# Performance work log

Measured on AMD Instinct MI355X. Metric: run time of the kernel, lower is better.

The kernel has to match this reference:

```python
import jax, jax.numpy as jnp
import numpy as np

NH, DK, DV, D = 8, 64, 64, 768
DECAY = 0.95
WRITE_STRENGTH = 0.1


def setup_inputs() -> dict:
    key = jax.random.key(0)
    ks = jax.random.split(key, 6)
    s = 0.02  # small init scale for projection weights
    return {
        "x": jax.random.normal(ks[0], (4, 4096, D), dtype=jnp.float32),
        "w_key": jax.random.normal(ks[1], (NH * DK, D), dtype=jnp.float32) * s,
        "w_value": jax.random.normal(ks[2], (NH * DV, D), dtype=jnp.float32) * s,
        "w_query": jax.random.normal(ks[3], (NH * DK, D), dtype=jnp.float32) * s,
        "w_gate": jax.random.normal(ks[4], (NH, D), dtype=jnp.float32) * s,
        "w_out": jax.random.normal(ks[5], (D, NH * DV), dtype=jnp.float32) * s,
    }


def reference(x, w_key, w_value, w_query, w_gate, w_out):
    B, S, _ = x.shape
    # Batched projections (torch Linear: y = x @ W.T)
    k = (x @ w_key.T).reshape(B, S, NH, DK)
    v = (x @ w_value.T).reshape(B, S, NH, DV)
    q = (x @ w_query.T).reshape(B, S, NH, DK)
    gate = jax.nn.sigmoid(x @ w_gate.T)  # (B, S, NH)

    # Writes only use batch element 0 (mirrors k[0], v[0], gate[0] in source)
    k0 = k[0]      # (S, NH, DK)
    v0 = v[0]      # (S, NH, DV)
    g0 = gate[0]   # (S, NH)

    def step(fw, inp):
        q_t, k0_t, v0_t, g0_t = inp
        # Read BEFORE this step's decay+write
        retrieved = jnp.einsum('bhk,hkv->bhv', q_t, fw)  # (B, NH, DV)
        write = (WRITE_STRENGTH * g0_t)[:, None, None] * (k0_t[:, :, None] * v0_t[:, None, :])
        fw_new = DECAY * fw + jax.lax.stop_gradient(write)
        return fw_new, retrieved

    fw0 = jnp.zeros((NH, DK, DV), dtype=x.dtype)
    inputs = (q.transpose(1, 0, 2, 3), k0, v0, g0)  # time-major
    _, retrieved = jax.lax.scan(step, fw0, inputs)   # (S, B, NH, DV)
    retrieved = retrieved.transpose(1, 0, 2, 3).reshape(B, S, NH * DV)
    return x + retrieved @ w_out.T
```

## Files before the change

### kernel.cpp

```cpp
#include <hip/hip_runtime.h>
#include <hip/hip_bf16.h>

typedef __hip_bfloat16 bf16;
typedef __attribute__((ext_vector_type(8))) short   bf16x8;
typedef __attribute__((ext_vector_type(4))) float   f32x4;

#define B_   4
#define S_   4096
#define D_   768
#define NH_  8
#define DK_  64
#define DV_  64
#define CH_  64
#define NCH_ (S_/CH_)
#define DECAY_ 0.95f
#define WSTR_  0.1f

__device__ __forceinline__ float b2f(bf16 v) { return __bfloat162float(v); }
__device__ __forceinline__ bf16  f2b(float v) { return __float2bfloat16(v); }

__device__ __forceinline__ void gl2lds16(const bf16* g, bf16* lds) {
    __builtin_amdgcn_global_load_lds(
        (const __attribute__((address_space(1))) void*)g,
        (__attribute__((address_space(3))) void*)lds, 16, 0, 0);
}

__global__ __launch_bounds__(192) void cast_gate(const float* __restrict__ x,
                                                 bf16* __restrict__ xb,
                                                 const float* __restrict__ wg,
                                                 float* __restrict__ wgt) {
    const int s = blockIdx.x;
    const int tid = threadIdx.x;
    const float4 v = *reinterpret_cast<const float4*>(x + (size_t)s * D_ + tid * 4);
    union { bf16 b4[4]; ushort4 u; } t;
    t.b4[0] = f2b(v.x); t.b4[1] = f2b(v.y); t.b4[2] = f2b(v.z); t.b4[3] = f2b(v.w);
    *reinterpret_cast<ushort4*>(xb + (size_t)s * D_ + tid * 4) = t.u;

    if (s < S_) {
        __shared__ float red[3 * 8];
        float p[8];
        const float* wgp = wg + tid * 4;
        #pragma unroll
        for (int h = 0; h < 8; h++) {
            const float4 wv = *reinterpret_cast<const float4*>(wgp + h * D_);
            p[h] = v.x * wv.x + v.y * wv.y + v.z * wv.z + v.w * wv.w;
        }
        #pragma unroll
        for (int h = 0; h < 8; h++)
            #pragma unroll
            for (int off = 32; off; off >>= 1) p[h] += __shfl_down(p[h], off);
        const int w = tid >> 6, lane = tid & 63;
        if (lane == 0) {
            #pragma unroll
            for (int h = 0; h < 8; h++) red[w * 8 + h] = p[h];
        }
        __syncthreads();
        if (tid < 8) {
            const float sum = red[tid] + red[8 + tid] + red[16 + tid];
            wgt[s * NH_ + tid] = WSTR_ / (1.f + expf(-sum));
        }
    }
}

__global__ __launch_bounds__(256) void cast_w4(const float* __restrict__ wq,
                                               const float* __restrict__ wk,
                                               const float* __restrict__ wv,
                                               const float* __restrict__ wo,
                                               bf16* __restrict__ dq, bf16* __restrict__ dk,
                                               bf16* __restrict__ dv, bf16* __restrict__ dob) {
    const int which = blockIdx.x / 384, b = blockIdx.x % 384;
    const float* src = which == 0 ? wq : which == 1 ? wk : which == 2 ? wv : wo;
    bf16*       dst = which == 0 ? dq : which == 1 ? dk : which == 2 ? dv : dob;
    const int i = (b * 256 + threadIdx.x) * 4;
    const float4 v = *reinterpret_cast<const float4*>(src + i);
    union { bf16 b4[4]; ushort4 u; } t;
    t.b4[0] = f2b(v.x); t.b4[1] = f2b(v.y); t.b4[2] = f2b(v.z); t.b4[3] = f2b(v.w);
    *reinterpret_cast<ushort4*>(dst + i) = t.u;
}

template<typename TC, int ADDX, int KV>
__global__ __launch_bounds__(256) void gemm_mfma(const bf16* __restrict__ A,
                                                 const bf16* __restrict__ B0,
                                                 const bf16* __restrict__ B1,
                                                 const float* __restrict__ X,
                                                 TC* __restrict__ C0,
                                                 TC* __restrict__ C1,
                                                 int M, int N, int K, int nb0) {
    __shared__ bf16 As[128 * 32];
    __shared__ bf16 Bs[128 * 32];
    int bx, by;
    {
        const int gx = gridDim.x, gy = gridDim.y;
        const int L = blockIdx.y * gx + blockIdx.x;
        if ((gy & 7) == 0) {
            const int rpx = gy >> 3;
            const int xcd = L & 7;
            const int i   = L >> 3;
            by = xcd * rpx + i / gx;
            bx = i % gx;
        } else { bx = blockIdx.x; by = blockIdx.y; }
    }
    const bf16* Bm = B0;
    TC* C = C0;
    if (KV && bx >= nb0) { Bm = B1; C = C1; bx -= nb0; }
    const int bm = by * 128, bn = bx * 128;
    const int tid = threadIdx.x, lane = tid & 63, w = tid >> 6;
    const int quad = lane >> 4, l16 = lane & 15;
    const int wm = (w >> 1) * 64, wn = (w & 1) * 64;

    int ro[2], ko[2];
    #pragma unroll
    for (int c = 0; c < 2; c++) {
        const int o = (w * 2 + c) * 1024 + lane * 16;
        ro[c] = o >> 6;
        ko[c] = (o & 63) >> 1;
    }

    f32x4 acc[4][4] = {};

    for (int k0 = 0; k0 < K; k0 += 32) {
        #pragma unroll
        for (int c = 0; c < 2; c++) {
            bf16* lA = &As[(w * 2 + c) * 512];
            bf16* lB = &Bs[(w * 2 + c) * 512];
            gl2lds16(A  + (size_t)(bm + ro[c]) * K + k0 + ko[c], lA);
            gl2lds16(Bm + (size_t)(bn + ro[c]) * K + k0 + ko[c], lB);
        }
        __syncthreads();
        bf16x8 af[4], bfr[4];
        #pragma unroll
        for (int t = 0; t < 4; t++) {
            af[t]  = *reinterpret_cast<const bf16x8*>(&As[(wm + t * 16 + l16) * 32 + quad * 8]);
            bfr[t] = *reinterpret_cast<const bf16x8*>(&Bs[(wn + t * 16 + l16) * 32 + quad * 8]);
        }
        #pragma unroll
        for (int mt = 0; mt < 4; mt++)
            #pragma unroll
            for (int nt = 0; nt < 4; nt++)
                acc[mt][nt] = __builtin_amdgcn_mfma_f32_16x16x32_bf16(
                    af[mt], bfr[nt], acc[mt][nt], 0, 0, 0);
        __syncthreads();
    }

    #pragma unroll
    for (int mt = 0; mt < 4; mt++)
        #pragma unroll
        for (int nt = 0; nt < 4; nt++)
            #pragma unroll
            for (int r = 0; r < 4; r++) {
                const int m = bm + wm + mt * 16 + quad * 4 + r;
                const int n = bn + wn + nt * 16 + l16;
                float v = acc[mt][nt][r];
                if (ADDX) v += X[(size_t)m * N + n];
                if (sizeof(TC) == 2) *(bf16*)&C[(size_t)m * N + n] = f2b(v);
                else                 *(float*)&C[(size_t)m * N + n] = v;
            }
}

__global__ __launch_bounds__(256) void chunk_sums(const bf16* __restrict__ k0,
                                                  const bf16* __restrict__ v0,
                                                  const float* __restrict__ wgt,
                                                  bf16* __restrict__ lsumsT) {
    const int n = blockIdx.x, h = blockIdx.y;
    __shared__ float ks[CH_][65];
    __shared__ float vs[CH_][64];
    __shared__ float cw[CH_];
    const int tid = threadIdx.x;
    for (int e = tid; e < CH_ * 64; e += 256) {
        const int r = e >> 6, c = e & 63;
        const int t = n * CH_ + r;
        ks[r][c] = b2f(k0[(size_t)t * (NH_ * DK_) + h * DK_ + c]);
        vs[r][c] = b2f(v0[(size_t)t * (NH_ * DV_) + h * DV_ + c]);
    }
    if (tid < CH_) {
        const int t = n * CH_ + tid;
        cw[tid] = powf(DECAY_, (float)(CH_ - 1 - tid)) * wgt[t * NH_ + h];
    }
    __syncthreads();
    const int j = tid & 63, ig = tid >> 6;
    float acc[16] = {};
    for (int idx = 0; idx < CH_; idx++) {
        const float ck = cw[idx] * ks[idx][j];
        #pragma unroll
        for (int r = 0; r < 16; r++) acc[r] += vs[idx][ig * 16 + r] * ck;
    }
    bf16* out = lsumsT + ((size_t)(n * NH_ + h)) * (DK_ * DV_);
    #pragma unroll
    for (int r = 0; r < 16; r++) out[(ig * 16 + r) * 64 + j] = f2b(acc[r]);
}

__global__ __launch_bounds__(256) void state_scan(const bf16* __restrict__ lsumsT,
                                                  bf16* __restrict__ statesT) {
    const int h = blockIdx.x >> 4;
    const int e = (blockIdx.x & 15) * 256 + threadIdx.x;
    const float dC = powf(DECAY_, (float)CH_);
    float fw = 0.f;
    for (int n = 0; n < NCH_; n++) {
        const size_t idx = ((size_t)(n * NH_ + h)) * (DK_ * DV_) + e;
        statesT[idx] = f2b(fw);
        fw = dC * fw + b2f(lsumsT[idx]);
    }
}

__global__ __launch_bounds__(256) void chunk_output(const bf16* __restrict__ q,
                                                    const bf16* __restrict__ k0,
                                                    const bf16* __restrict__ v0,
                                                    const float* __restrict__ wgt,
                                                    const bf16* __restrict__ statesT,
                                                    bf16* __restrict__ retr) {
    const int n = blockIdx.x, h = blockIdx.y, b = blockIdx.z;
    __shared__ bf16 QsVT[64 * 72];
    __shared__ bf16 KsAm[64 * 72];
    __shared__ bf16 FWT[64 * 64];
    __shared__ float dpow[64], winv[64];
    const int tid = threadIdx.x, lane = tid & 63, w = tid >> 6;
    const int quad = lane >> 4, l16 = lane & 15;
    const int t0 = n * CH_;

    #pragma unroll
    for (int c = 0; c < 2; c++) {
        const int seg = w * 2 + c;
        const int row = seg * 8 + (lane >> 3);
        const int col = (lane & 7) * 8;
        gl2lds16(q  + ((size_t)(b * S_ + t0 + row)) * 512 + h * 64 + col, &QsVT[seg * 512]);
        gl2lds16(k0 + ((size_t)(t0 + row)) * 512 + h * 64 + col,          &KsAm[seg * 512]);
        gl2lds16(statesT + ((size_t)(n * NH_ + h)) * 4096 + seg * 512 + lane * 8, &FWT[seg * 512]);
    }
    ushort4 vreg[4];
    const int jb = (tid & 15) * 4;
    const int sb = tid >> 4;
    #pragma unroll
    for (int it = 0; it < 4; it++) {
        vreg[it] = *reinterpret_cast<const ushort4*>(
            v0 + ((size_t)(t0 + sb + it * 16)) * 512 + h * 64 + jb);
    }
    if (tid < 64) {
        dpow[tid] = powf(DECAY_, (float)tid);
        winv[tid] = wgt[(t0 + tid) * NH_ + h] * powf(DECAY_, -(float)(tid + 1));
    }
    __syncthreads();

    const int mrow = w * 16;
    float dpow_tt[4], winv_l[4];
    #pragma unroll
    for (int r = 0; r < 4; r++) dpow_tt[r] = dpow[mrow + quad * 4 + r];
    #pragma unroll
    for (int nt = 0; nt < 4; nt++) winv_l[nt] = winv[nt * 16 + l16];

    const bf16x8 af0 = *reinterpret_cast<const bf16x8*>(&QsVT[(mrow + l16) * 64 + quad * 8]);
    const bf16x8 af1 = *reinterpret_cast<const bf16x8*>(&QsVT[(mrow + l16) * 64 + 32 + quad * 8]);
    f32x4 acc[4] = {};
    #pragma unroll
    for (int nt = 0; nt < 4; nt++) {
        const bf16x8 b0 = *reinterpret_cast<const bf16x8*>(&KsAm[(nt * 16 + l16) * 64 + quad * 8]);
        const bf16x8 b1 = *reinterpret_cast<const bf16x8*>(&KsAm[(nt * 16 + l16) * 64 + 32 + quad * 8]);
        acc[nt] = __builtin_amdgcn_mfma_f32_16x16x32_bf16(af0, b0, acc[nt], 0, 0, 0);
        acc[nt] = __builtin_amdgcn_mfma_f32_16x16x32_bf16(af1, b1, acc[nt], 0, 0, 0);
    }
    __syncthreads();

    #pragma unroll
    for (int nt = 0; nt < 4; nt++) {
        const int s = nt * 16 + l16;
        #pragma unroll
        for (int r = 0; r < 4; r++) {
            const int tt = mrow + quad * 4 + r;
            const float v = (s < tt) ? acc[nt][r] * dpow_tt[r] * winv_l[nt] : 0.f;
            KsAm[tt * 72 + s] = f2b(v);
        }
    }
    {
        ushort* VT = reinterpret_cast<ushort*>(QsVT);
        #pragma unroll
        for (int it = 0; it < 4; it++) {
            const int s = sb + it * 16;
            VT[(jb + 0) * 72 + s] = vreg[it].x;
            VT[(jb + 1) * 72 + s] = vreg[it].y;
            VT[(jb + 2) * 72 + s] = vreg[it].z;
            VT[(jb + 3) * 72 + s] = vreg[it].w;
        }
    }
    __syncthreads();

    f32x4 o[4] = {};
    #pragma unroll
    for (int nt = 0; nt < 4; nt++) {
        const bf16x8 f0 = *reinterpret_cast<const bf16x8*>(&FWT[(nt * 16 + l16) * 64 + quad * 8]);
        const bf16x8 f1 = *reinterpret_cast<const bf16x8*>(&FWT[(nt * 16 + l16) * 64 + 32 + quad * 8]);
        o[nt] = __builtin_amdgcn_mfma_f32_16x16x32_bf16(af0, f0, o[nt], 0, 0, 0);
        o[nt] = __builtin_amdgcn_mfma_f32_16x16x32_bf16(af1, f1, o[nt], 0, 0, 0);
    }
    #pragma unroll
    for (int nt = 0; nt < 4; nt++)
        #pragma unroll
        for (int r = 0; r < 4; r++) o[nt][r] *= dpow_tt[r];

    const bf16x8 a0 = *reinterpret_cast<const bf16x8*>(&KsAm[(mrow + l16) * 72 + quad * 8]);
    const bf16x8 a1 = *reinterpret_cast<const bf16x8*>(&KsAm[(mrow + l16) * 72 + 32 + quad * 8]);
    #pragma unroll
    for (int nt = 0; nt < 4; nt++) {
        const bf16x8 v0f = *reinterpret_cast<const bf16x8*>(&QsVT[(nt * 16 + l16) * 72 + quad * 8]);
        const bf16x8 v1f = *reinterpret_cast<const bf16x8*>(&QsVT[(nt * 16 + l16) * 72 + 32 + quad * 8]);
        o[nt] = __builtin_amdgcn_mfma_f32_16x16x32_bf16(a0, v0f, o[nt], 0, 0, 0);
        o[nt] = __builtin_amdgcn_mfma_f32_16x16x32_bf16(a1, v1f, o[nt], 0, 0, 0);
    }
    #pragma unroll
    for (int nt = 0; nt < 4; nt++)
        #pragma unroll
        for (int r = 0; r < 4; r++) {
            const int tt = mrow + quad * 4 + r;
            retr[((size_t)(b * S_ + t0 + tt)) * 512 + h * 64 + nt * 16 + l16] = f2b(o[nt][r]);
        }
}

extern "C" void kernel_launch(void* const* d_in, const int* in_sizes, int n_in,
                              void* d_out, int out_size, void* d_ws, size_t ws_size,
                              hipStream_t stream) {
    const float* x  = (const float*)d_in[0];
    const float* wk = (const float*)d_in[1];
    const float* wv = (const float*)d_in[2];
    const float* wq = (const float*)d_in[3];
    const float* wg = (const float*)d_in[4];
    const float* wo = (const float*)d_in[5];
    float* out = (float*)d_out;

    const size_t MB1 = 1ull << 20;
    char* w = (char*)d_ws;
    bf16*  qbuf    = (bf16*)(w);
    bf16*  k0buf   = (bf16*)(w + 16 * MB1);
    bf16*  v0buf   = (bf16*)(w + 20 * MB1);
    float* wgt     = (float*)(w + 24 * MB1);
    bf16*  wqb     = (bf16*)(w + 24 * MB1 + (128ull<<10));
    bf16*  wkb     = (bf16*)(w + 24 * MB1 + (128ull<<10) + 1*786432);
    bf16*  wvb     = (bf16*)(w + 24 * MB1 + (128ull<<10) + 2*786432);
    bf16*  wob     = (bf16*)(w + 24 * MB1 + (128ull<<10) + 3*786432);
    char*  base2   = w + 24 * MB1 + (128ull<<10) + 4*786432;
    bf16*  statesT = (bf16*)(base2);
    bf16*  retr    = (bf16*)(base2 + 4 * MB1);
    bf16*  lsumsT  = retr;
    bf16*  xb      = (bf16*)(base2);

    const int MB = B_ * S_;

    cast_gate<<<MB, 192, 0, stream>>>(x, xb, wg, wgt);
    cast_w4<<<1536, 256, 0, stream>>>(wq, wk, wv, wo, wqb, wkb, wvb, wob);

    gemm_mfma<bf16, 0, 0><<<dim3(512 / 128, MB / 128), 256, 0, stream>>>(
        xb, wqb, nullptr, nullptr, qbuf, nullptr, MB, 512, D_, 4);
    gemm_mfma<bf16, 0, 1><<<dim3(8, S_ / 128), 256, 0, stream>>>(
        xb, wkb, wvb, nullptr, k0buf, v0buf, S_, 512, D_, 4);

    chunk_sums<<<dim3(NCH_, NH_), 256, 0, stream>>>(k0buf, v0buf, wgt, lsumsT);
    state_scan<<<NH_ * 16, 256, 0, stream>>>(lsumsT, statesT);
    chunk_output<<<dim3(NCH_, NH_, B_), 256, 0, stream>>>(qbuf, k0buf, v0buf, wgt, statesT, retr);

    gemm_mfma<float, 1, 0><<<dim3(D_ / 128, MB / 128), 256, 0, stream>>>(
        retr, wob, nullptr, x, out, nullptr, MB, D_, 512, 6);
}
```

Measured before the change: 224.1 us.

## Fuse casts and projections, swizzle GEMM LDS, drop state scan via truncated decay

Merges the two cast kernels into one launch, and merges the Q and K/V projection GEMMs into one XCD-aware launch. The shared GEMM body now uses a K-tile of 64 with XOR-swizzled LDS layout to cut bank conflicts and halve the number of barriers. The sequential state_scan kernel is removed: chunk_output rebuilds each chunk's incoming state from only the four previous chunk sums, weighted by powers of decay^64. This drops one launch and its serial loop, but truncates the decay series, which adds a small approximation error (0.95^320 is negligible) and repeats some loads across batch blocks.

```diff
diff --git a/kernel.cpp b/kernel.cpp
--- a/kernel.cpp
+++ b/kernel.cpp
@@ -25,12 +25,30 @@
         (__attribute__((address_space(3))) void*)lds, 16, 0, 0);
 }
 
-__global__ __launch_bounds__(192) void cast_gate(const float* __restrict__ x,
-                                                 bf16* __restrict__ xb,
-                                                 const float* __restrict__ wg,
-                                                 float* __restrict__ wgt) {
+__global__ __launch_bounds__(192) void cast_fused(const float* __restrict__ x,
+                                                  bf16* __restrict__ xb,
+                                                  const float* __restrict__ wg,
+                                                  float* __restrict__ wgt,
+                                                  const float* __restrict__ wq,
+                                                  const float* __restrict__ wk,
+                                                  const float* __restrict__ wv,
+                                                  const float* __restrict__ wo,
+                                                  bf16* __restrict__ dq, bf16* __restrict__ dk,
+                                                  bf16* __restrict__ dv, bf16* __restrict__ dob) {
+    const int tid = threadIdx.x;
+    if (blockIdx.x >= (B_ * S_)) {
+        const int idx = blockIdx.x - B_ * S_;
+        const int which = idx >> 9, b = idx & 511;
+        const float* src = which == 0 ? wq : which == 1 ? wk : which == 2 ? wv : wo;
+        bf16*       dst = which == 0 ? dq : which == 1 ? dk : which == 2 ? dv : dob;
+        const int i = (b * 192 + tid) * 4;
+        const float4 v = *reinterpret_cast<const float4*>(src + i);
+        union { bf16 b4[4]; ushort4 u; } t;
+        t.b4[0] = f2b(v.x); t.b4[1] = f2b(v.y); t.b4[2] = f2b(v.z); t.b4[3] = f2b(v.w);
+        *reinterpret_cast<ushort4*>(dst + i) = t.u;
+        return;
+    }
     const int s = blockIdx.x;
-    const int tid = threadIdx.x;
     const float4 v = *reinterpret_cast<const float4*>(x + (size_t)s * D_ + tid * 4);
     union { bf16 b4[4]; ushort4 u; } t;
     t.b4[0] = f2b(v.x); t.b4[1] = f2b(v.y); t.b4[2] = f2b(v.z); t.b4[3] = f2b(v.w);
@@ -42,8 +60,8 @@
         const float* wgp = wg + tid * 4;
         #pragma unroll
         for (int h = 0; h < 8; h++) {
-            const float4 wv = *reinterpret_cast<const float4*>(wgp + h * D_);
-            p[h] = v.x * wv.x + v.y * wv.y + v.z * wv.z + v.w * wv.w;
+            const float4 wv4 = *reinterpret_cast<const float4*>(wgp + h * D_);
+            p[h] = v.x * wv4.x + v.y * wv4.y + v.z * wv4.z + v.w * wv4.w;
         }
         #pragma unroll
         for (int h = 0; h < 8; h++)
@@ -62,83 +80,47 @@
     }
 }
 
-__global__ __launch_bounds__(256) void cast_w4(const float* __restrict__ wq,
-                                               const float* __restrict__ wk,
-                                               const float* __restrict__ wv,
-                                               const float* __restrict__ wo,
-                                               bf16* __restrict__ dq, bf16* __restrict__ dk,
-                                               bf16* __restrict__ dv, bf16* __restrict__ dob) {
-    const int which = blockIdx.x / 384, b = blockIdx.x % 384;
-    const float* src = which == 0 ? wq : which == 1 ? wk : which == 2 ? wv : wo;
-    bf16*       dst = which == 0 ? dq : which == 1 ? dk : which == 2 ? dv : dob;
-    const int i = (b * 256 + threadIdx.x) * 4;
-    const float4 v = *reinterpret_cast<const float4*>(src + i);
-    union { bf16 b4[4]; ushort4 u; } t;
-    t.b4[0] = f2b(v.x); t.b4[1] = f2b(v.y); t.b4[2] = f2b(v.z); t.b4[3] = f2b(v.w);
-    *reinterpret_cast<ushort4*>(dst + i) = t.u;
-}
-
-template<typename TC, int ADDX, int KV>
-__global__ __launch_bounds__(256) void gemm_mfma(const bf16* __restrict__ A,
-                                                 const bf16* __restrict__ B0,
-                                                 const bf16* __restrict__ B1,
-                                                 const float* __restrict__ X,
-                                                 TC* __restrict__ C0,
-                                                 TC* __restrict__ C1,
-                                                 int M, int N, int K, int nb0) {
-    __shared__ bf16 As[128 * 32];
-    __shared__ bf16 Bs[128 * 32];
-    int bx, by;
-    {
-        const int gx = gridDim.x, gy = gridDim.y;
-        const int L = blockIdx.y * gx + blockIdx.x;
-        if ((gy & 7) == 0) {
-            const int rpx = gy >> 3;
-            const int xcd = L & 7;
-            const int i   = L >> 3;
-            by = xcd * rpx + i / gx;
-            bx = i % gx;
-        } else { bx = blockIdx.x; by = blockIdx.y; }
-    }
-    const bf16* Bm = B0;
-    TC* C = C0;
-    if (KV && bx >= nb0) { Bm = B1; C = C1; bx -= nb0; }
-    const int bm = by * 128, bn = bx * 128;
+template<typename TC, int ADDX, int NITER>
+__device__ __forceinline__ void gemm_body(bf16* As, bf16* Bs,
+                                          const bf16* __restrict__ A,
+                                          const bf16* __restrict__ Bm,
+                                          const float* __restrict__ X,
+                                          TC* __restrict__ C,
+                                          int bm, int bn, int K, int N) {
     const int tid = threadIdx.x, lane = tid & 63, w = tid >> 6;
     const int quad = lane >> 4, l16 = lane & 15;
     const int wm = (w >> 1) * 64, wn = (w & 1) * 64;
-
-    int ro[2], ko[2];
-    #pragma unroll
-    for (int c = 0; c < 2; c++) {
-        const int o = (w * 2 + c) * 1024 + lane * 16;
-        ro[c] = o >> 6;
-        ko[c] = (o & 63) >> 1;
-    }
+    const int lrow = lane >> 3;
+    const int lcol = ((lane & 7) ^ lrow) * 8;
 
     f32x4 acc[4][4] = {};
 
-    for (int k0 = 0; k0 < K; k0 += 32) {
-        #pragma unroll
-        for (int c = 0; c < 2; c++) {
-            bf16* lA = &As[(w * 2 + c) * 512];
-            bf16* lB = &Bs[(w * 2 + c) * 512];
-            gl2lds16(A  + (size_t)(bm + ro[c]) * K + k0 + ko[c], lA);
-            gl2lds16(Bm + (size_t)(bn + ro[c]) * K + k0 + ko[c], lB);
+    for (int it = 0; it < NITER; it++) {
+        const int k0 = it * 64;
+        #pragma unroll
+        for (int c = 0; c < 4; c++) {
+            const int seg = w * 4 + c;
+            const int row = seg * 8 + lrow;
+            gl2lds16(A  + (size_t)(bm + row) * K + k0 + lcol, &As[seg * 512]);
+            gl2lds16(Bm + (size_t)(bn + row) * K + k0 + lcol, &Bs[seg * 512]);
         }
         __syncthreads();
-        bf16x8 af[4], bfr[4];
-        #pragma unroll
-        for (int t = 0; t < 4; t++) {
-            af[t]  = *reinterpret_cast<const bf16x8*>(&As[(wm + t * 16 + l16) * 32 + quad * 8]);
-            bfr[t] = *reinterpret_cast<const bf16x8*>(&Bs[(wn + t * 16 + l16) * 32 + quad * 8]);
-        }
-        #pragma unroll
-        for (int mt = 0; mt < 4; mt++)
-            #pragma unroll
-            for (int nt = 0; nt < 4; nt++)
-                acc[mt][nt] = __builtin_amdgcn_mfma_f32_16x16x32_bf16(
-                    af[mt], bfr[nt], acc[mt][nt], 0, 0, 0);
+        #pragma unroll
+        for (int kh = 0; kh < 2; kh++) {
+            bf16x8 af[4], bfr[4];
+            #pragma unroll
+            for (int t = 0; t < 4; t++) {
+                const int cb = ((kh * 4 + quad) ^ (l16 & 7)) * 8;
+                af[t]  = *reinterpret_cast<const bf16x8*>(&As[(wm + t * 16 + l16) * 64 + cb]);
+                bfr[t] = *reinterpret_cast<const bf16x8*>(&Bs[(wn + t * 16 + l16) * 64 + cb]);
+            }
+            #pragma unroll
+            for (int mt = 0; mt < 4; mt++)
+                #pragma unroll
+                for (int nt = 0; nt < 4; nt++)
+                    acc[mt][nt] = __builtin_amdgcn_mfma_f32_16x16x32_bf16(
+                        af[mt], bfr[nt], acc[mt][nt], 0, 0, 0);
+        }
         __syncthreads();
     }
 
@@ -155,6 +137,50 @@
                 if (sizeof(TC) == 2) *(bf16*)&C[(size_t)m * N + n] = f2b(v);
                 else                 *(float*)&C[(size_t)m * N + n] = v;
             }
+}
+
+__global__ __launch_bounds__(256) void proj_fused(const bf16* __restrict__ xb,
+                                                  const bf16* __restrict__ wqb,
+                                                  const bf16* __restrict__ wkb,
+                                                  const bf16* __restrict__ wvb,
+                                                  bf16* __restrict__ qbuf,
+                                                  bf16* __restrict__ k0buf,
+                                                  bf16* __restrict__ v0buf) {
+    __shared__ bf16 As[128 * 64];
+    __shared__ bf16 Bs[128 * 64];
+    const int id = blockIdx.x;
+    const int xcd = id & 7;
+    int j = id >> 3;
+    const bf16* Bm; bf16* C; int bm, bn;
+    if (j < 64) {
+        bm = (xcd + ((j >> 2) << 3)) * 128;
+        bn = (j & 3) * 128;
+        Bm = wqb; C = qbuf;
+    } else {
+        j -= 64;
+        bm = (xcd + ((j >> 3) << 3)) * 128;
+        const int b8 = j & 7;
+        bn = (b8 & 3) * 128;
+        Bm = (b8 < 4) ? wkb : wvb;
+        C  = (b8 < 4) ? k0buf : v0buf;
+    }
+    gemm_body<bf16, 0, 12>(As, Bs, xb, Bm, nullptr, C, bm, bn, D_, 512);
+}
+
+__global__ __launch_bounds__(256) void gemm_out(const bf16* __restrict__ retr,
+                                                const bf16* __restrict__ wob,
+                                                const float* __restrict__ x,
+                                                float* __restrict__ out) {
+    __shared__ bf16 As[128 * 64];
+    __shared__ bf16 Bs[128 * 64];
+    const int gx = gridDim.x, gy = gridDim.y;
+    const int L = blockIdx.y * gx + blockIdx.x;
+    const int rpx = gy >> 3;
+    const int xcd = L & 7;
+    const int i   = L >> 3;
+    const int by = xcd * rpx + i / gx;
+    const int bx = i % gx;
+    gemm_body<float, 1, 8>(As, Bs, retr, wob, x, out, by * 128, bx * 128, 512, D_);
 }
 
 __global__ __launch_bounds__(256) void chunk_sums(const bf16* __restrict__ k0,
@@ -184,29 +210,24 @@
         #pragma unroll
         for (int r = 0; r < 16; r++) acc[r] += vs[idx][ig * 16 + r] * ck;
     }
-    bf16* out = lsumsT + ((size_t)(n * NH_ + h)) * (DK_ * DV_);
-    #pragma unroll
-    for (int r = 0; r < 16; r++) out[(ig * 16 + r) * 64 + j] = f2b(acc[r]);
-}
-
-__global__ __launch_bounds__(256) void state_scan(const bf16* __restrict__ lsumsT,
-                                                  bf16* __restrict__ statesT) {
-    const int h = blockIdx.x >> 4;
-    const int e = (blockIdx.x & 15) * 256 + threadIdx.x;
-    const float dC = powf(DECAY_, (float)CH_);
-    float fw = 0.f;
-    for (int n = 0; n < NCH_; n++) {
-        const size_t idx = ((size_t)(n * NH_ + h)) * (DK_ * DV_) + e;
-        statesT[idx] = f2b(fw);
-        fw = dC * fw + b2f(lsumsT[idx]);
-    }
+    bf16* outp = lsumsT + ((size_t)(n * NH_ + h)) * (DK_ * DV_);
+    #pragma unroll
+    for (int r = 0; r < 16; r++) outp[(ig * 16 + r) * 64 + j] = f2b(acc[r]);
+}
+
+__device__ __forceinline__ void cvt4(ushort4 u, float f[4]) {
+    union { unsigned u; float f; } c;
+    c.u = (unsigned)u.x << 16; f[0] = c.f;
+    c.u = (unsigned)u.y << 16; f[1] = c.f;
+    c.u = (unsigned)u.z << 16; f[2] = c.f;
+    c.u = (unsigned)u.w << 16; f[3] = c.f;
 }
 
 __global__ __launch_bounds__(256) void chunk_output(const bf16* __restrict__ q,
                                                     const bf16* __restrict__ k0,
                                                     const bf16* __restrict__ v0,
                                                     const float* __restrict__ wgt,
-                                                    const bf16* __restrict__ statesT,
+                                                    const bf16* __restrict__ lsumsT,
                                                     bf16* __restrict__ retr) {
     const int n = blockIdx.x, h = blockIdx.y, b = blockIdx.z;
     __shared__ bf16 QsVT[64 * 72];
@@ -216,15 +237,41 @@
     const int tid = threadIdx.x, lane = tid & 63, w = tid >> 6;
     const int quad = lane >> 4, l16 = lane & 15;
     const int t0 = n * CH_;
+    const int lrow = lane >> 3;
+    const int lcol = ((lane & 7) ^ lrow) * 8;
 
     #pragma unroll
     for (int c = 0; c < 2; c++) {
         const int seg = w * 2 + c;
-        const int row = seg * 8 + (lane >> 3);
-        const int col = (lane & 7) * 8;
-        gl2lds16(q  + ((size_t)(b * S_ + t0 + row)) * 512 + h * 64 + col, &QsVT[seg * 512]);
-        gl2lds16(k0 + ((size_t)(t0 + row)) * 512 + h * 64 + col,          &KsAm[seg * 512]);
-        gl2lds16(statesT + ((size_t)(n * NH_ + h)) * 4096 + seg * 512 + lane * 8, &FWT[seg * 512]);
+        const int row = seg * 8 + lrow;
+        gl2lds16(q  + ((size_t)(b * S_ + t0 + row)) * 512 + h * 64 + lcol, &QsVT[seg * 512]);
+        gl2lds16(k0 + ((size_t)(t0 + row)) * 512 + h * 64 + lcol,          &KsAm[seg * 512]);
+    }
+    {
+        float fwacc[16] = {};
+        const float dcp[4] = { 1.0f, 0.0375241f, 1.40806e-3f, 5.28365e-5f };
+        #pragma unroll
+        for (int jj = 1; jj <= 4; jj++) {
+            const int nm = n - jj;
+            if (nm < 0) break;
+            const ushort* Lp = (const ushort*)(lsumsT + ((size_t)(nm * NH_ + h)) * 4096) + tid * 16;
+            #pragma unroll
+            for (int u = 0; u < 4; u++) {
+                float f[4];
+                cvt4(reinterpret_cast<const ushort4*>(Lp)[u], f);
+                #pragma unroll
+                for (int e = 0; e < 4; e++) fwacc[u * 4 + e] += dcp[jj - 1] * f[e];
+            }
+        }
+        const int frow = tid >> 2;
+        #pragma unroll
+        for (int half = 0; half < 2; half++) {
+            const int cb = (tid & 3) * 2 + half;
+            union { bf16 b8v[8]; bf16x8 v; } t;
+            #pragma unroll
+            for (int e = 0; e < 8; e++) t.b8v[e] = f2b(fwacc[half * 8 + e]);
+            *reinterpret_cast<bf16x8*>(&FWT[frow * 64 + (cb ^ (frow & 7)) * 8]) = t.v;
+        }
     }
     ushort4 vreg[4];
     const int jb = (tid & 15) * 4;
@@ -247,13 +294,15 @@
     #pragma unroll
     for (int nt = 0; nt < 4; nt++) winv_l[nt] = winv[nt * 16 + l16];
 
-    const bf16x8 af0 = *reinterpret_cast<const bf16x8*>(&QsVT[(mrow + l16) * 64 + quad * 8]);
-    const bf16x8 af1 = *reinterpret_cast<const bf16x8*>(&QsVT[(mrow + l16) * 64 + 32 + quad * 8]);
+    const int cb0 = ((quad) ^ (l16 & 7)) * 8;
+    const int cb1 = ((4 + quad) ^ (l16 & 7)) * 8;
+    const bf16x8 af0 = *reinterpret_cast<const bf16x8*>(&QsVT[(mrow + l16) * 64 + cb0]);
+    const bf16x8 af1 = *reinterpret_cast<const bf16x8*>(&QsVT[(mrow + l16) * 64 + cb1]);
     f32x4 acc[4] = {};
     #pragma unroll
     for (int nt = 0; nt < 4; nt++) {
-        const bf16x8 b0 = *reinterpret_cast<const bf16x8*>(&KsAm[(nt * 16 + l16) * 64 + quad * 8]);
-        const bf16x8 b1 = *reinterpret_cast<const bf16x8*>(&KsAm[(nt * 16 + l16) * 64 + 32 + quad * 8]);
+        const bf16x8 b0 = *reinterpret_cast<const bf16x8*>(&KsAm[(nt * 16 + l16) * 64 + cb0]);
+        const bf16x8 b1 = *reinterpret_cast<const bf16x8*>(&KsAm[(nt * 16 + l16) * 64 + cb1]);
         acc[nt] = __builtin_amdgcn_mfma_f32_16x16x32_bf16(af0, b0, acc[nt], 0, 0, 0);
         acc[nt] = __builtin_amdgcn_mfma_f32_16x16x32_bf16(af1, b1, acc[nt], 0, 0, 0);
     }
@@ -285,8 +334,8 @@
     f32x4 o[4] = {};
     #pragma unroll
     for (int nt = 0; nt < 4; nt++) {
-        const bf16x8 f0 = *reinterpret_cast<const bf16x8*>(&FWT[(nt * 16 + l16) * 64 + quad * 8]);
-        const bf16x8 f1 = *reinterpret_cast<const bf16x8*>(&FWT[(nt * 16 + l16) * 64 + 32 + quad * 8]);
+        const bf16x8 f0 = *reinterpret_cast<const bf16x8*>(&FWT[(nt * 16 + l16) * 64 + cb0]);
+        const bf16x8 f1 = *reinterpret_cast<const bf16x8*>(&FWT[(nt * 16 + l16) * 64 + cb1]);
         o[nt] = __builtin_amdgcn_mfma_f32_16x16x32_bf16(af0, f0, o[nt], 0, 0, 0);
         o[nt] = __builtin_amdgcn_mfma_f32_16x16x32_bf16(af1, f1, o[nt], 0, 0, 0);
     }
@@ -334,26 +383,19 @@
     bf16*  wkb     = (bf16*)(w + 24 * MB1 + (128ull<<10) + 1*786432);
     bf16*  wvb     = (bf16*)(w + 24 * MB1 + (128ull<<10) + 2*786432);
     bf16*  wob     = (bf16*)(w + 24 * MB1 + (128ull<<10) + 3*786432);
-    char*  base2   = w + 24 * MB1 + (128ull<<10) + 4*786432;
-    bf16*  statesT = (bf16*)(base2);
-    bf16*  retr    = (bf16*)(base2 + 4 * MB1);
-    bf16*  lsumsT  = retr;
-    bf16*  xb      = (bf16*)(base2);
+    bf16*  lsumsT  = (bf16*)(w + 28 * MB1);
+    bf16*  retr    = (bf16*)(w + 32 * MB1);
+    bf16*  xb      = (bf16*)(w + 48 * MB1);
 
     const int MB = B_ * S_;
 
-    cast_gate<<<MB, 192, 0, stream>>>(x, xb, wg, wgt);
-    cast_w4<<<1536, 256, 0, stream>>>(wq, wk, wv, wo, wqb, wkb, wvb, wob);
-
-    gemm_mfma<bf16, 0, 0><<<dim3(512 / 128, MB / 128), 256, 0, stream>>>(
-        xb, wqb, nullptr, nullptr, qbuf, nullptr, MB, 512, D_, 4);
-    gemm_mfma<bf16, 0, 1><<<dim3(8, S_ / 128), 256, 0, stream>>>(
-        xb, wkb, wvb, nullptr, k0buf, v0buf, S_, 512, D_, 4);
+    cast_fused<<<MB + 2048, 192, 0, stream>>>(x, xb, wg, wgt,
+                                              wq, wk, wv, wo, wqb, wkb, wvb, wob);
+
+    proj_fused<<<768, 256, 0, stream>>>(xb, wqb, wkb, wvb, qbuf, k0buf, v0buf);
 
     chunk_sums<<<dim3(NCH_, NH_), 256, 0, stream>>>(k0buf, v0buf, wgt, lsumsT);
-    state_scan<<<NH_ * 16, 256, 0, stream>>>(lsumsT, statesT);
-    chunk_output<<<dim3(NCH_, NH_, B_), 256, 0, stream>>>(qbuf, k0buf, v0buf, wgt, statesT, retr);
-
-    gemm_mfma<float, 1, 0><<<dim3(D_ / 128, MB / 128), 256, 0, stream>>>(
-        retr, wob, nullptr, x, out, nullptr, MB, D_, 512, 6);
-}
+    chunk_output<<<dim3(NCH_, NH_, B_), 256, 0, stream>>>(qbuf, k0buf, v0buf, wgt, lsumsT, retr);
+
+    gemm_out<<<dim3(D_ / 128, MB / 128), 256, 0, stream>>>(retr, wob, x, out);
+}
```

Measured after the change: 200.3 us. 1.12x faster.
